# Optimization experiments

Hardware: AMD Instinct MI355X
Metric: run time of the kernel (lower is better)

Reference implementation:

```python
import jax, jax.numpy as jnp
import numpy as np

N, K, IN_C, OUT_C, EDGE_D = 50000, 32, 128, 64, 32
E = N * K
MSG_EPS = 1e-7
BN_EPS = 1e-5


def setup_inputs() -> dict:
    rng = np.random.default_rng(0)
    # Consistent graph: edge e has destination e // K; nbr[n] lists n's edges, -1-padded.
    nbr = np.arange(E, dtype=np.int64).reshape(N, K)
    deg = rng.integers(K // 2, K + 1, size=N)
    nbr = np.where(np.arange(K)[None, :] < deg[:, None], nbr, -1)
    dst = np.repeat(np.arange(N, dtype=np.int64), K)
    src = rng.integers(0, N, size=E).astype(np.int64)
    edge_index = np.stack([src, dst])

    key = jax.random.key(0)
    ks = jax.random.split(key, 8)
    init = lambda k, shape, fan: (jax.random.normal(k, shape, jnp.float32) / np.sqrt(fan)).astype(jnp.float32)
    return {
        "x": jax.random.normal(ks[0], (N, IN_C), jnp.float32),
        "edge_attr": jax.random.normal(ks[1], (E, EDGE_D), jnp.float32),
        "w_src": init(ks[2], (OUT_C, IN_C), IN_C),
        "w_dst": init(ks[3], (OUT_C, IN_C), IN_C),
        "w_edge": init(ks[4], (OUT_C, EDGE_D), EDGE_D),
        "w1": init(ks[5], (2 * OUT_C, OUT_C), OUT_C),
        "gamma": jnp.ones((2 * OUT_C,), jnp.float32),
        "beta": jnp.zeros((2 * OUT_C,), jnp.float32),
        "w2": init(ks[6], (OUT_C, 2 * OUT_C), 2 * OUT_C),
        "edge_index": jnp.asarray(edge_index),
        "nbr": jnp.asarray(nbr),
    }


def _gather_sum(src, nbr_idx, valid):
    # src: [E,H] per-edge values; nbr_idx: [N,K] clamped edge ids; valid: [N,K]
    g = src[nbr_idx]                                   # [N,K,H]
    return jnp.where(valid[..., None], g, 0.0).sum(axis=1)  # [N,H]


def reference(x, edge_attr, w_src, w_dst, w_edge, w1, gamma, beta, w2, edge_index, nbr):
    valid = nbr >= 0
    nidx = jnp.clip(nbr, 0)
    src_n, dest = edge_index[0], edge_index[1]

    src = x @ w_src.T                                  # [N,H]
    dst_feat = x @ w_dst.T                             # [N,H]
    x_j = src[src_n]                                   # [E,H]
    msg = jax.nn.relu(x_j + edge_attr @ w_edge.T) + MSG_EPS  # [E,H]

    # softmax over each destination's neighbor edges (gather-max / gather-sum via nbr)
    neg = -jnp.finfo(msg.dtype).max
    gmax = jnp.where(valid[..., None], msg[nidx], neg).max(axis=1)   # [N,H]
    alpha = jnp.exp(msg - gmax[dest])                                # [E,H]
    denom = _gather_sum(alpha, nidx, valid) + 1e-16                  # [N,H]
    alpha = alpha / denom[dest]

    out = _gather_sum(msg * alpha, nidx, valid) + dst_feat           # [N,H]

    # MLP: Linear -> BatchNorm1d(train-mode batch stats, biased var) -> ReLU -> Linear
    h = out @ w1.T                                     # [N,2H]
    mean = h.mean(axis=0)
    var = h.var(axis=0)
    h = (h - mean) * jax.lax.rsqrt(var + BN_EPS) * gamma + beta
    h = jax.nn.relu(h)
    return h @ w2.T                                    # [N,H]
```

## Files before the change

### kernel.cpp

```cpp
#include <hip/hip_runtime.h>
#include <hip/hip_bf16.h>
#include <float.h>

#define NN 50000
#define KNB 32
#define INC 128
#define HC 64
#define EDD 32
#define H2C 128
#define NBLK 782

typedef __attribute__((ext_vector_type(8))) short bf16x8;
typedef __attribute__((ext_vector_type(4))) float f32x4;

__device__ __forceinline__ short f2bf(float f) {
    unsigned u = __builtin_bit_cast(unsigned, f);
    u += 0x7fffu + ((u >> 16) & 1u);
    return (short)(u >> 16);
}
__device__ __forceinline__ float bf2f(short h) {
    unsigned u = ((unsigned)(unsigned short)h) << 16;
    return __builtin_bit_cast(float, u);
}

__global__ __launch_bounds__(256) void k_prep(
    const float* __restrict__ w_src, const float* __restrict__ w_dst,
    const float* __restrict__ w1, const float* __restrict__ w2,
    const float* __restrict__ w_edge,
    short* __restrict__ pAhi, short* __restrict__ pAlo,
    short* __restrict__ p1hi, short* __restrict__ p1lo,
    short* __restrict__ p2hi, short* __restrict__ p2lo,
    short* __restrict__ pE)
{
    const int tid = blockIdx.x * 256 + threadIdx.x;
    const int nT  = gridDim.x * 256;
    for (int idx = tid; idx < 16384; idx += nT) {
        int kt = (idx >> 12) & 3, nt = (idx >> 9) & 7, lane = (idx >> 3) & 63, j = idx & 7;
        int lr = lane & 15, lg = lane >> 4;
        int ch = nt * 16 + lr, k = kt * 32 + lg * 8 + j;
        float f = (ch < 64) ? w_src[ch * 128 + k] : w_dst[(ch - 64) * 128 + k];
        short hi = f2bf(f);
        pAhi[idx] = hi; pAlo[idx] = f2bf(f - bf2f(hi));
    }
    for (int idx = tid; idx < 8192; idx += nT) {
        int kt = (idx >> 12) & 1, nt = (idx >> 9) & 7, lane = (idx >> 3) & 63, j = idx & 7;
        int lr = lane & 15, lg = lane >> 4;
        int ch = nt * 16 + lr, k = kt * 32 + lg * 8 + j;
        float f = w1[ch * 64 + k];
        short hi = f2bf(f);
        p1hi[idx] = hi; p1lo[idx] = f2bf(f - bf2f(hi));
    }
    for (int idx = tid; idx < 8192; idx += nT) {
        int kt = (idx >> 11) & 3, nt = (idx >> 9) & 3, lane = (idx >> 3) & 63, j = idx & 7;
        int lr = lane & 15, lg = lane >> 4;
        int ch = nt * 16 + lr, k = kt * 32 + lg * 8 + j;
        float f = w2[ch * 128 + k];
        short hi = f2bf(f);
        p2hi[idx] = hi; p2lo[idx] = f2bf(f - bf2f(hi));
    }
    for (int idx = tid; idx < 2048; idx += nT) {
        int nt = (idx >> 9) & 3, lane = (idx >> 3) & 63, j = idx & 7;
        int lr = lane & 15, lg = lane >> 4;
        int ch = nt * 16 + lr, k = lg * 8 + j;
        pE[idx] = f2bf(w_edge[ch * EDD + k]);
    }
}

__device__ __forceinline__ void split8(const float* av, bf16x8& ahi, bf16x8& alo) {
    #pragma unroll
    for (int j = 0; j < 8; ++j) {
        short h = f2bf(av[j]);
        ahi[j] = h;
        alo[j] = f2bf(av[j] - bf2f(h));
    }
}

__global__ __launch_bounds__(256) void k_lin1(
    const float* __restrict__ x, const short* __restrict__ pAhi,
    const short* __restrict__ pAlo, float* __restrict__ srcP,
    float* __restrict__ dstf)
{
    const int lane = threadIdx.x & 63, wave = threadIdx.x >> 6;
    const int lr = lane & 15, lg = lane >> 4;
    const int nb = blockIdx.x * 64 + wave * 16;
    const bf16x8* Bh = (const bf16x8*)pAhi;
    const bf16x8* Bl = (const bf16x8*)pAlo;
    int row = nb + lr; if (row > NN - 1) row = NN - 1;

    f32x4 acc[8];
    #pragma unroll
    for (int i = 0; i < 8; ++i) acc[i] = (f32x4){0.f, 0.f, 0.f, 0.f};

    #pragma unroll
    for (int kt = 0; kt < 4; ++kt) {
        const float* ap = x + (size_t)row * INC + kt * 32 + lg * 8;
        float4 a0 = *(const float4*)ap, a1 = *(const float4*)(ap + 4);
        float av[8] = {a0.x, a0.y, a0.z, a0.w, a1.x, a1.y, a1.z, a1.w};
        bf16x8 ahi, alo;
        split8(av, ahi, alo);
        #pragma unroll
        for (int nt = 0; nt < 8; ++nt) {
            bf16x8 bh = Bh[(kt * 8 + nt) * 64 + lane];
            bf16x8 bl = Bl[(kt * 8 + nt) * 64 + lane];
            acc[nt] = __builtin_amdgcn_mfma_f32_16x16x32_bf16(ahi, bl, acc[nt], 0, 0, 0);
            acc[nt] = __builtin_amdgcn_mfma_f32_16x16x32_bf16(alo, bh, acc[nt], 0, 0, 0);
            acc[nt] = __builtin_amdgcn_mfma_f32_16x16x32_bf16(ahi, bh, acc[nt], 0, 0, 0);
        }
    }
    #pragma unroll
    for (int nt = 0; nt < 8; ++nt)
        #pragma unroll
        for (int q = 0; q < 4; ++q) {
            int node = nb + lg * 4 + q;
            if (node < NN) {
                float v = acc[nt][q];
                if (nt < 4) srcP[node * HC + lr * 4 + nt] = v;
                else        dstf[node * HC + (nt - 4) * 16 + lr] = v;
            }
        }
}

__global__ __launch_bounds__(256) void k_edge_agg_mfma(
    const float* __restrict__ srcP, const float* __restrict__ dstf,
    const float* __restrict__ edge_attr, const short* __restrict__ pE,
    const int* __restrict__ esrc, const int* __restrict__ nbr,
    float* __restrict__ outf)
{
    const int lane = threadIdx.x & 63;
    const int wave = threadIdx.x >> 6;
    const int n    = blockIdx.x * 4 + wave;

    const int lr = lane & 15;
    const int lg = lane >> 4;

    int4 sv0 = *(const int4*)&esrc[n * KNB + lg * 4];
    int4 sv1 = *(const int4*)&esrc[n * KNB + 16 + lg * 4];
    int sidx[2][4] = {{sv0.x, sv0.y, sv0.z, sv0.w}, {sv1.x, sv1.y, sv1.z, sv1.w}};

    int nbv = nbr[n * KNB + (lane & 31)];
    unsigned long long bm = __ballot((lane < 32) && (nbv >= 0));
    unsigned int vmask = (unsigned int)bm;

    float4 xjv[2][4];
    #pragma unroll
    for (int mt = 0; mt < 2; ++mt)
        #pragma unroll
        for (int r = 0; r < 4; ++r)
            xjv[mt][r] = *(const float4*)&srcP[(size_t)sidx[mt][r] * HC + lr * 4];

    const float* ab = edge_attr + (size_t)n * KNB * EDD;
    bf16x8 afrag[2];
    #pragma unroll
    for (int mt = 0; mt < 2; ++mt) {
        const float* ap = ab + (mt * 16 + lr) * EDD + lg * 8;
        float4 a0 = *(const float4*)ap;
        float4 a1 = *(const float4*)(ap + 4);
        float av[8] = {a0.x, a0.y, a0.z, a0.w, a1.x, a1.y, a1.z, a1.w};
        bf16x8 dummy;
        split8(av, afrag[mt], dummy);
        (void)dummy;
    }

    const bf16x8* Bp = (const bf16x8*)pE;
    bf16x8 bfrag[4];
    #pragma unroll
    for (int nt = 0; nt < 4; ++nt) bfrag[nt] = Bp[nt * 64 + lane];

    f32x4 p[2][4];
    #pragma unroll
    for (int mt = 0; mt < 2; ++mt)
        #pragma unroll
        for (int nt = 0; nt < 4; ++nt) {
            f32x4 z = {0.f, 0.f, 0.f, 0.f};
            p[mt][nt] = __builtin_amdgcn_mfma_f32_16x16x32_bf16(
                afrag[mt], bfrag[nt], z, 0, 0, 0);
        }

    float msg[2][4][4];
    float vf[2][4];
    #pragma unroll
    for (int mt = 0; mt < 2; ++mt)
        #pragma unroll
        for (int r = 0; r < 4; ++r) {
            int k = mt * 16 + lg * 4 + r;
            vf[mt][r] = ((vmask >> k) & 1u) ? 1.f : 0.f;
            float xj[4] = {xjv[mt][r].x, xjv[mt][r].y, xjv[mt][r].z, xjv[mt][r].w};
            #pragma unroll
            for (int nt = 0; nt < 4; ++nt) {
                float m = p[mt][nt][r] + xj[nt];
                msg[mt][r][nt] = fmaxf(m, 0.f) + 1e-7f;
            }
        }

    float res[4];
    #pragma unroll
    for (int nt = 0; nt < 4; ++nt) {
        float lm = -FLT_MAX;
        #pragma unroll
        for (int mt = 0; mt < 2; ++mt)
            #pragma unroll
            for (int r = 0; r < 4; ++r) {
                float v = (vf[mt][r] > 0.f) ? msg[mt][r][nt] : -FLT_MAX;
                lm = fmaxf(lm, v);
            }
        lm = fmaxf(lm, __shfl_xor(lm, 16, 64));
        lm = fmaxf(lm, __shfl_xor(lm, 32, 64));
        float se = 0.f, ws = 0.f;
        #pragma unroll
        for (int mt = 0; mt < 2; ++mt)
            #pragma unroll
            for (int r = 0; r < 4; ++r) {
                float t = __expf(msg[mt][r][nt] - lm) * vf[mt][r];
                se += t;
                ws += msg[mt][r][nt] * t;
            }
        se += __shfl_xor(se, 16, 64); ws += __shfl_xor(ws, 16, 64);
        se += __shfl_xor(se, 32, 64); ws += __shfl_xor(ws, 32, 64);
        res[nt] = ws / (se + 1e-16f);
    }

    float r01 = (lg & 1) ? res[1] : res[0];
    float r23 = (lg & 1) ? res[3] : res[2];
    float rr  = (lg & 2) ? r23 : r01;
    outf[n * HC + lane] = rr + dstf[n * HC + lane];
}

__global__ __launch_bounds__(256) void k_lin2(
    const float* __restrict__ outf, const short* __restrict__ p1hi,
    const short* __restrict__ p1lo, float* __restrict__ h,
    float* __restrict__ partials)
{
    __shared__ float ps[128 * 16], pq[128 * 16];
    const int t = threadIdx.x;
    const int lane = t & 63, wave = t >> 6;
    const int lr = lane & 15, lg = lane >> 4;
    const int nb = blockIdx.x * 64 + wave * 16;
    const bf16x8* Bh = (const bf16x8*)p1hi;
    const bf16x8* Bl = (const bf16x8*)p1lo;
    int row = nb + lr; if (row > NN - 1) row = NN - 1;

    f32x4 acc[8];
    #pragma unroll
    for (int i = 0; i < 8; ++i) acc[i] = (f32x4){0.f, 0.f, 0.f, 0.f};

    #pragma unroll
    for (int kt = 0; kt < 2; ++kt) {
        const float* ap = outf + (size_t)row * HC + kt * 32 + lg * 8;
        float4 a0 = *(const float4*)ap, a1 = *(const float4*)(ap + 4);
        float av[8] = {a0.x, a0.y, a0.z, a0.w, a1.x, a1.y, a1.z, a1.w};
        bf16x8 ahi, alo;
        split8(av, ahi, alo);
        #pragma unroll
        for (int nt = 0; nt < 8; ++nt) {
            bf16x8 bh = Bh[(kt * 8 + nt) * 64 + lane];
            bf16x8 bl = Bl[(kt * 8 + nt) * 64 + lane];
            acc[nt] = __builtin_amdgcn_mfma_f32_16x16x32_bf16(ahi, bl, acc[nt], 0, 0, 0);
            acc[nt] = __builtin_amdgcn_mfma_f32_16x16x32_bf16(alo, bh, acc[nt], 0, 0, 0);
            acc[nt] = __builtin_amdgcn_mfma_f32_16x16x32_bf16(ahi, bh, acc[nt], 0, 0, 0);
        }
    }

    #pragma unroll
    for (int nt = 0; nt < 8; ++nt) {
        float s = 0.f, q = 0.f;
        #pragma unroll
        for (int qq = 0; qq < 4; ++qq) {
            int node = nb + lg * 4 + qq;
            float v = acc[nt][qq];
            if (node < NN) {
                h[node * H2C + nt * 16 + lr] = v;
                s += v;
                q += v * v;
            }
        }
        ps[(nt * 16 + lr) * 16 + wave * 4 + lg] = s;
        pq[(nt * 16 + lr) * 16 + wave * 4 + lg] = q;
    }
    __syncthreads();
    if (t < 128) {
        float s = 0.f, q = 0.f;
        #pragma unroll
        for (int i = 0; i < 16; ++i) { s += ps[t * 16 + i]; q += pq[t * 16 + i]; }
        partials[blockIdx.x * 256 + t]       = s;
        partials[blockIdx.x * 256 + 128 + t] = q;
    }
}

__global__ __launch_bounds__(1024) void k_bn_finalize(
    const float* __restrict__ partials, int nblk,
    const float* __restrict__ gamma, const float* __restrict__ beta,
    float* __restrict__ sb)
{
    const int t = threadIdx.x;
    const int f = t & 63;
    const int g = t >> 6;

    float4 acc = {0.f, 0.f, 0.f, 0.f};
    for (int b = g; b < nblk; b += 16) {
        float4 v = *(const float4*)&partials[b * 256 + f * 4];
        acc.x += v.x; acc.y += v.y; acc.z += v.z; acc.w += v.w;
    }

    __shared__ __align__(16) float4 red[16][64];
    red[g][f] = acc;
    __syncthreads();
    #pragma unroll
    for (int s = 8; s > 0; s >>= 1) {
        if (g < s) {
            float4 o = red[g + s][f];
            acc.x += o.x; acc.y += o.y; acc.z += o.z; acc.w += o.w;
            red[g][f] = acc;
        }
        __syncthreads();
    }

    if (t < 128) {
        const float* row = (const float*)&red[0][0];
        float s = row[t];
        float q = row[128 + t];
        float mean = s / (float)NN;
        float var  = q / (float)NN - mean * mean;
        float scale = gamma[t] * rsqrtf(var + 1e-5f);
        float bias  = beta[t] - mean * scale;
        sb[t]       = scale;
        sb[128 + t] = bias;
    }
}

__global__ __launch_bounds__(256) void k_lin3(
    const float* __restrict__ h, const short* __restrict__ p2hi,
    const short* __restrict__ p2lo, const float* __restrict__ sb,
    float* __restrict__ out)
{
    const int lane = threadIdx.x & 63, wave = threadIdx.x >> 6;
    const int lr = lane & 15, lg = lane >> 4;
    const int nb = blockIdx.x * 64 + wave * 16;
    const bf16x8* Bh = (const bf16x8*)p2hi;
    const bf16x8* Bl = (const bf16x8*)p2lo;
    int row = nb + lr; if (row > NN - 1) row = NN - 1;

    f32x4 acc[4];
    #pragma unroll
    for (int i = 0; i < 4; ++i) acc[i] = (f32x4){0.f, 0.f, 0.f, 0.f};

    #pragma unroll
    for (int kt = 0; kt < 4; ++kt) {
        const int k0 = kt * 32 + lg * 8;
        float4 sc0 = *(const float4*)&sb[k0],       sc1 = *(const float4*)&sb[k0 + 4];
        float4 bi0 = *(const float4*)&sb[128 + k0], bi1 = *(const float4*)&sb[128 + k0 + 4];
        const float* ap = h + (size_t)row * H2C + k0;
        float4 a0 = *(const float4*)ap, a1 = *(const float4*)(ap + 4);
        float av[8]  = {a0.x, a0.y, a0.z, a0.w, a1.x, a1.y, a1.z, a1.w};
        float scv[8] = {sc0.x, sc0.y, sc0.z, sc0.w, sc1.x, sc1.y, sc1.z, sc1.w};
        float biv[8] = {bi0.x, bi0.y, bi0.z, bi0.w, bi1.x, bi1.y, bi1.z, bi1.w};
        float rv[8];
        #pragma unroll
        for (int j = 0; j < 8; ++j) {
            float v = av[j] * scv[j] + biv[j];
            rv[j] = v > 0.f ? v : 0.f;
        }
        bf16x8 ahi, alo;
        split8(rv, ahi, alo);
        #pragma unroll
        for (int nt = 0; nt < 4; ++nt) {
            bf16x8 bh = Bh[(kt * 4 + nt) * 64 + lane];
            bf16x8 bl = Bl[(kt * 4 + nt) * 64 + lane];
            acc[nt] = __builtin_amdgcn_mfma_f32_16x16x32_bf16(ahi, bl, acc[nt], 0, 0, 0);
            acc[nt] = __builtin_amdgcn_mfma_f32_16x16x32_bf16(alo, bh, acc[nt], 0, 0, 0);
            acc[nt] = __builtin_amdgcn_mfma_f32_16x16x32_bf16(ahi, bh, acc[nt], 0, 0, 0);
        }
    }
    #pragma unroll
    for (int nt = 0; nt < 4; ++nt)
        #pragma unroll
        for (int q = 0; q < 4; ++q) {
            int node = nb + lg * 4 + q;
            if (node < NN) out[node * HC + nt * 16 + lr] = acc[nt][q];
        }
}

extern "C" void kernel_launch(void* const* d_in, const int* in_sizes, int n_in,
                              void* d_out, int out_size, void* d_ws, size_t ws_size,
                              hipStream_t stream) {
    const float* x         = (const float*)d_in[0];
    const float* edge_attr = (const float*)d_in[1];
    const float* w_src     = (const float*)d_in[2];
    const float* w_dst     = (const float*)d_in[3];
    const float* w_edge    = (const float*)d_in[4];
    const float* w1        = (const float*)d_in[5];
    const float* gamma     = (const float*)d_in[6];
    const float* beta      = (const float*)d_in[7];
    const float* w2        = (const float*)d_in[8];
    const int*   eidx      = (const int*)d_in[9];
    const int*   nbr       = (const int*)d_in[10];

    float* ws   = (float*)d_ws;
    float* srcP = ws;
    float* dstf = ws + 3200000;
    float* outf = ws + 6400000;
    float* h    = ws + 9600000;
    float* part = ws + 16000000;
    float* sb   = ws + 16250000;
    short* sp   = (short*)(ws + 16300000);
    short* pAhi = sp;
    short* pAlo = sp + 16384;
    short* p1hi = sp + 32768;
    short* p1lo = sp + 40960;
    short* p2hi = sp + 49152;
    short* p2lo = sp + 57344;
    short* pE   = sp + 65536;

    hipLaunchKernelGGL(k_prep,          dim3(32),    dim3(256),  0, stream,
                       w_src, w_dst, w1, w2, w_edge,
                       pAhi, pAlo, p1hi, p1lo, p2hi, p2lo, pE);
    hipLaunchKernelGGL(k_lin1,          dim3(NBLK),  dim3(256),  0, stream,
                       x, pAhi, pAlo, srcP, dstf);
    hipLaunchKernelGGL(k_edge_agg_mfma, dim3(12500), dim3(256),  0, stream,
                       srcP, dstf, edge_attr, pE, eidx, nbr, outf);
    hipLaunchKernelGGL(k_lin2,          dim3(NBLK),  dim3(256),  0, stream,
                       outf, p1hi, p1lo, h, part);
    hipLaunchKernelGGL(k_bn_finalize,   dim3(1),     dim3(1024), 0, stream,
                       part, NBLK, gamma, beta, sb);
    hipLaunchKernelGGL(k_lin3,          dim3(NBLK),  dim3(256),  0, stream,
                       h, p2hi, p2lo, sb, (float*)d_out);
}
```

Measured before the change: 152.6 us.

## Process two destination nodes per wave and drop softmax max pass

```diff
diff --git a/kernel.cpp b/kernel.cpp
--- a/kernel.cpp
+++ b/kernel.cpp
@@ -128,101 +128,112 @@
 {
     const int lane = threadIdx.x & 63;
     const int wave = threadIdx.x >> 6;
-    const int n    = blockIdx.x * 4 + wave;
-
-    const int lr = lane & 15;
-    const int lg = lane >> 4;
-
-    int4 sv0 = *(const int4*)&esrc[n * KNB + lg * 4];
-    int4 sv1 = *(const int4*)&esrc[n * KNB + 16 + lg * 4];
-    int sidx[2][4] = {{sv0.x, sv0.y, sv0.z, sv0.w}, {sv1.x, sv1.y, sv1.z, sv1.w}};
-
-    int nbv = nbr[n * KNB + (lane & 31)];
-    unsigned long long bm = __ballot((lane < 32) && (nbv >= 0));
-    unsigned int vmask = (unsigned int)bm;
-
-    float4 xjv[2][4];
-    #pragma unroll
-    for (int mt = 0; mt < 2; ++mt)
-        #pragma unroll
-        for (int r = 0; r < 4; ++r)
-            xjv[mt][r] = *(const float4*)&srcP[(size_t)sidx[mt][r] * HC + lr * 4];
-
-    const float* ab = edge_attr + (size_t)n * KNB * EDD;
-    bf16x8 afrag[2];
-    #pragma unroll
-    for (int mt = 0; mt < 2; ++mt) {
-        const float* ap = ab + (mt * 16 + lr) * EDD + lg * 8;
-        float4 a0 = *(const float4*)ap;
-        float4 a1 = *(const float4*)(ap + 4);
-        float av[8] = {a0.x, a0.y, a0.z, a0.w, a1.x, a1.y, a1.z, a1.w};
-        bf16x8 dummy;
-        split8(av, afrag[mt], dummy);
-        (void)dummy;
-    }
+    const int n0   = (blockIdx.x * 4 + wave) * 2;
+    const int n1   = n0 + 1;
+    const int lr = lane & 15, lg = lane >> 4;
+
+    int4 s00 = *(const int4*)&esrc[n0 * KNB + lg * 4];
+    int4 s01 = *(const int4*)&esrc[n0 * KNB + 16 + lg * 4];
+    int4 s10 = *(const int4*)&esrc[n1 * KNB + lg * 4];
+    int4 s11 = *(const int4*)&esrc[n1 * KNB + 16 + lg * 4];
+    int nbv0 = nbr[n0 * KNB + (lane & 31)];
+    int nbv1 = nbr[n1 * KNB + (lane & 31)];
+    float d0 = dstf[n0 * HC + lane];
+    float d1 = dstf[n1 * HC + lane];
 
     const bf16x8* Bp = (const bf16x8*)pE;
     bf16x8 bfrag[4];
     #pragma unroll
     for (int nt = 0; nt < 4; ++nt) bfrag[nt] = Bp[nt * 64 + lane];
 
-    f32x4 p[2][4];
-    #pragma unroll
-    for (int mt = 0; mt < 2; ++mt)
-        #pragma unroll
-        for (int nt = 0; nt < 4; ++nt) {
-            f32x4 z = {0.f, 0.f, 0.f, 0.f};
-            p[mt][nt] = __builtin_amdgcn_mfma_f32_16x16x32_bf16(
-                afrag[mt], bfrag[nt], z, 0, 0, 0);
-        }
-
-    float msg[2][4][4];
-    float vf[2][4];
-    #pragma unroll
-    for (int mt = 0; mt < 2; ++mt)
-        #pragma unroll
-        for (int r = 0; r < 4; ++r) {
-            int k = mt * 16 + lg * 4 + r;
-            vf[mt][r] = ((vmask >> k) & 1u) ? 1.f : 0.f;
-            float xj[4] = {xjv[mt][r].x, xjv[mt][r].y, xjv[mt][r].z, xjv[mt][r].w};
+    const float* ab0 = edge_attr + (size_t)n0 * KNB * EDD;
+    const float* ab1 = edge_attr + (size_t)n1 * KNB * EDD;
+    float4 at0[4], at1[4];
+    #pragma unroll
+    for (int mt = 0; mt < 2; ++mt) {
+        at0[mt * 2]     = *(const float4*)(ab0 + (mt * 16 + lr) * EDD + lg * 8);
+        at0[mt * 2 + 1] = *(const float4*)(ab0 + (mt * 16 + lr) * EDD + lg * 8 + 4);
+        at1[mt * 2]     = *(const float4*)(ab1 + (mt * 16 + lr) * EDD + lg * 8);
+        at1[mt * 2 + 1] = *(const float4*)(ab1 + (mt * 16 + lr) * EDD + lg * 8 + 4);
+    }
+
+    int i00[4] = {s00.x, s00.y, s00.z, s00.w};
+    int i01[4] = {s01.x, s01.y, s01.z, s01.w};
+    int i10[4] = {s10.x, s10.y, s10.z, s10.w};
+    int i11[4] = {s11.x, s11.y, s11.z, s11.w};
+    float4 xj0[2][4], xj1[2][4];
+    #pragma unroll
+    for (int r = 0; r < 4; ++r) {
+        xj0[0][r] = *(const float4*)&srcP[(size_t)i00[r] * HC + lr * 4];
+        xj0[1][r] = *(const float4*)&srcP[(size_t)i01[r] * HC + lr * 4];
+    }
+    #pragma unroll
+    for (int r = 0; r < 4; ++r) {
+        xj1[0][r] = *(const float4*)&srcP[(size_t)i10[r] * HC + lr * 4];
+        xj1[1][r] = *(const float4*)&srcP[(size_t)i11[r] * HC + lr * 4];
+    }
+
+    unsigned long long bm0 = __ballot((lane < 32) && (nbv0 >= 0));
+    unsigned long long bm1 = __ballot((lane < 32) && (nbv1 >= 0));
+    unsigned vm0 = (unsigned)bm0, vm1 = (unsigned)bm1;
+
+    float out0, out1;
+    #pragma unroll
+    for (int node = 0; node < 2; ++node) {
+        const float4* at = node ? at1 : at0;
+        const float4 (*xj)[4] = node ? xj1 : xj0;
+        unsigned vmask = node ? vm1 : vm0;
+
+        bf16x8 afrag[2];
+        #pragma unroll
+        for (int mt = 0; mt < 2; ++mt) {
+            float av[8] = {at[mt*2].x, at[mt*2].y, at[mt*2].z, at[mt*2].w,
+                           at[mt*2+1].x, at[mt*2+1].y, at[mt*2+1].z, at[mt*2+1].w};
+            bf16x8 lo;
+            split8(av, afrag[mt], lo);
+            (void)lo;
+        }
+
+        f32x4 p[2][4];
+        #pragma unroll
+        for (int mt = 0; mt < 2; ++mt)
             #pragma unroll
             for (int nt = 0; nt < 4; ++nt) {
-                float m = p[mt][nt][r] + xj[nt];
-                msg[mt][r][nt] = fmaxf(m, 0.f) + 1e-7f;
+                f32x4 z = {0.f, 0.f, 0.f, 0.f};
+                p[mt][nt] = __builtin_amdgcn_mfma_f32_16x16x32_bf16(
+                    afrag[mt], bfrag[nt], z, 0, 0, 0);
             }
-        }
-
-    float res[4];
-    #pragma unroll
-    for (int nt = 0; nt < 4; ++nt) {
-        float lm = -FLT_MAX;
-        #pragma unroll
-        for (int mt = 0; mt < 2; ++mt)
+
+        float res[4];
+        #pragma unroll
+        for (int nt = 0; nt < 4; ++nt) {
+            float se = 0.f, ws = 0.f;
             #pragma unroll
-            for (int r = 0; r < 4; ++r) {
-                float v = (vf[mt][r] > 0.f) ? msg[mt][r][nt] : -FLT_MAX;
-                lm = fmaxf(lm, v);
-            }
-        lm = fmaxf(lm, __shfl_xor(lm, 16, 64));
-        lm = fmaxf(lm, __shfl_xor(lm, 32, 64));
-        float se = 0.f, ws = 0.f;
-        #pragma unroll
-        for (int mt = 0; mt < 2; ++mt)
-            #pragma unroll
-            for (int r = 0; r < 4; ++r) {
-                float t = __expf(msg[mt][r][nt] - lm) * vf[mt][r];
-                se += t;
-                ws += msg[mt][r][nt] * t;
-            }
-        se += __shfl_xor(se, 16, 64); ws += __shfl_xor(ws, 16, 64);
-        se += __shfl_xor(se, 32, 64); ws += __shfl_xor(ws, 32, 64);
-        res[nt] = ws / (se + 1e-16f);
-    }
-
-    float r01 = (lg & 1) ? res[1] : res[0];
-    float r23 = (lg & 1) ? res[3] : res[2];
-    float rr  = (lg & 2) ? r23 : r01;
-    outf[n * HC + lane] = rr + dstf[n * HC + lane];
+            for (int mt = 0; mt < 2; ++mt)
+                #pragma unroll
+                for (int r = 0; r < 4; ++r) {
+                    float xjv = (nt == 0) ? xj[mt][r].x : (nt == 1) ? xj[mt][r].y
+                              : (nt == 2) ? xj[mt][r].z : xj[mt][r].w;
+                    float m = fmaxf(p[mt][nt][r] + xjv, 0.f) + 1e-7f;
+                    int k = mt * 16 + lg * 4 + r;
+                    float a = ((vmask >> k) & 1u) ? m : -FLT_MAX;
+                    float t = __expf(a);
+                    se += t;
+                    ws = fmaf(m, t, ws);
+                }
+            se += __shfl_xor(se, 16, 64); ws += __shfl_xor(ws, 16, 64);
+            se += __shfl_xor(se, 32, 64); ws += __shfl_xor(ws, 32, 64);
+            res[nt] = ws / (se + 1e-16f);
+        }
+
+        float r01 = (lg & 1) ? res[1] : res[0];
+        float r23 = (lg & 1) ? res[3] : res[2];
+        float rr  = (lg & 2) ? r23 : r01;
+        if (node == 0) out0 = rr; else out1 = rr;
+    }
+
+    outf[n0 * HC + lane] = out0 + d0;
+    outf[n1 * HC + lane] = out1 + d1;
 }
 
 __global__ __launch_bounds__(256) void k_lin2(
@@ -415,7 +426,7 @@
                        pAhi, pAlo, p1hi, p1lo, p2hi, p2lo, pE);
     hipLaunchKernelGGL(k_lin1,          dim3(NBLK),  dim3(256),  0, stream,
                        x, pAhi, pAlo, srcP, dstf);
-    hipLaunchKernelGGL(k_edge_agg_mfma, dim3(12500), dim3(256),  0, stream,
+    hipLaunchKernelGGL(k_edge_agg_mfma, dim3(6250),  dim3(256),  0, stream,
                        srcP, dstf, edge_attr, pE, eidx, nbr, outf);
     hipLaunchKernelGGL(k_lin2,          dim3(NBLK),  dim3(256),  0, stream,
                        outf, p1hi, p1lo, h, part);
```

Result: no change. 155.6 us (+2.0%).
